# Kernel tuning notes

Hardware: AMD Instinct MI355X
Metric: run time of the kernel (lower is better)

## Reference

```python
import jax, jax.numpy as jnp
import numpy as np

N_OUT = 100000 - 1  # 99999, as hard-coded in the torch module
LEAK = 0.01         # torch LeakyReLU default slope


def setup_inputs() -> dict:
    key = jax.random.key(0)
    k1, k2, k3, k4, k5 = jax.random.split(key, 5)
    B, D = 512, 512
    H = D // 2
    x = jax.random.normal(k1, (B, D), dtype=jnp.float32)
    # torch.nn.Linear-style init scale ~ 1/sqrt(fan_in)
    w2 = jax.random.normal(k2, (H, D), dtype=jnp.float32) / np.sqrt(D)
    b2 = jax.random.normal(k3, (H,), dtype=jnp.float32) / np.sqrt(D)
    w3 = jax.random.normal(k4, (55, H), dtype=jnp.float32) / np.sqrt(H)
    b3 = jax.random.normal(k5, (55,), dtype=jnp.float32) / np.sqrt(H)
    return {"x": x, "w2": w2, "b2": b2, "w3": w3, "b3": b3}


def _digit_tables():
    # Static integer tables for i in [0, N_OUT).
    i = np.arange(N_OUT, dtype=np.int32)
    ndig = ((i >= 10).astype(np.int32) + (i >= 100) + (i >= 1000) + (i >= 10000)).astype(np.int32)
    ndig[0] = 1  # special case in the original code: i==0 -> n=1
    return jnp.asarray(i), jnp.asarray(ndig)


def reference(x, w2, b2, w3, b3):
    # tiny MLP (batched; equivalent to the per-sample torch loop)
    h = x @ w2.T + b2
    h = jnp.where(h >= 0, h, LEAK * h)          # LeakyReLU
    z = h @ w3.T + b3                            # [B, 55]
    p_len = jax.nn.softmax(z[:, :5], axis=-1)    # length distribution (5)
    p_dig = jax.nn.softmax(z[:, 5:].reshape(-1, 5, 10), axis=-1)  # 5 digit groups of 10
    x3 = jnp.concatenate([p_len, p_dig.reshape(-1, 50)], axis=-1)  # [B, 55]

    i, ndig = _digit_tables()                    # [N], [N]
    out = jnp.take(x3, ndig, axis=1)             # lead factor x3[k, n_i] -> [B, N]
    # Multiply the first n_i digit probabilities (original drops the last digit).
    for j in range(4):                           # max usable digits: n<=4
        expo = jnp.maximum(ndig - j, 0)
        d = (i // jnp.power(10, expo)) % 10      # j-th most significant digit
        idx = 5 + d + 10 * j                     # index into x3 digit groups
        factor = jnp.take(x3, idx, axis=1)       # [B, N]
        valid = (j < ndig)[None, :]
        out = out * jnp.where(valid, factor, 1.0)
    return out
```

## Files before the change

kernel.cpp:

```cpp
#include <hip/hip_runtime.h>
#include <hip/hip_bf16.h>


#define BATCH 512
#define DIM   512
#define HID   256
#define NCLS  55
#define NOUT  99999
#define RPB   4
#define LEAK  0.01f

__global__ __launch_bounds__(256) void mlp_x3_kernel(
    const float* __restrict__ x,  const float* __restrict__ w2,
    const float* __restrict__ b2, const float* __restrict__ w3,
    const float* __restrict__ b3, float* __restrict__ x3out) {
    __shared__ float xs[RPB][DIM];
    __shared__ float hs[RPB][HID];
    __shared__ float zs[RPB][NCLS];

    const int tid = threadIdx.x;
    const int k0  = blockIdx.x * RPB;

    for (int idx = tid; idx < RPB * DIM; idx += 256) {
        int r = idx >> 9;
        int d = idx & (DIM - 1);
        xs[r][d] = x[(k0 + r) * DIM + d];
    }
    __syncthreads();

    float acc[RPB];
#pragma unroll
    for (int r = 0; r < RPB; ++r) acc[r] = 0.f;
    const float* w2row = w2 + tid * DIM;
#pragma unroll 4
    for (int d = 0; d < DIM; ++d) {
        float w = w2row[d];
#pragma unroll
        for (int r = 0; r < RPB; ++r) acc[r] += w * xs[r][d];
    }
    float bb = b2[tid];
#pragma unroll
    for (int r = 0; r < RPB; ++r) {
        float hv = acc[r] + bb;
        hs[r][tid] = (hv >= 0.f) ? hv : LEAK * hv;
    }
    __syncthreads();

    if (tid < RPB * NCLS) {
        int r = tid / NCLS, o = tid % NCLS;
        const float* w3row = w3 + o * HID;
        float a = b3[o];
#pragma unroll 4
        for (int d = 0; d < HID; ++d) a += hs[r][d] * w3row[d];
        zs[r][o] = a;
    }
    __syncthreads();

    if (tid < RPB * 6) {
        int r = tid / 6, g = tid % 6;
        int off = (g == 0) ? 0 : 5 + 10 * (g - 1);
        int len = (g == 0) ? 5 : 10;
        float m = -1e30f;
        for (int u = 0; u < len; ++u) m = fmaxf(m, zs[r][off + u]);
        float s = 0.f;
        for (int u = 0; u < len; ++u) {
            float e = __expf(zs[r][off + u] - m);
            zs[r][off + u] = e;
            s += e;
        }
        float inv = 1.f / s;
        float* orow = x3out + (k0 + r) * NCLS + off;
        for (int u = 0; u < len; ++u) orow[u] = zs[r][off + u] * inv;
    }
}

__global__ __launch_bounds__(256) void expand_kernel(
    const float* __restrict__ x3, float* __restrict__ out, int ngroups) {
    int g = blockIdx.x * 256 + threadIdx.x;
    if (g >= ngroups) return;
    unsigned e0 = (unsigned)g * 4u;
    float vv[4];
#pragma unroll
    for (int u = 0; u < 4; ++u) {
        unsigned e = e0 + (unsigned)u;
        unsigned k = e / 99999u;
        unsigned i = e - k * 99999u;
        const float* row = x3 + k * (unsigned)NCLS;
        unsigned nd = (i >= 10u) + (i >= 100u) + (i >= 1000u) + (i >= 10000u);
        if (i == 0u) nd = 1u;
        float v;
        unsigned d1, d2, d3, d4, r;
        switch (nd) {
            case 0:
                v = row[0];
                break;
            case 1:
                d1 = i / 10u;
                v = row[1] * row[5 + d1];
                break;
            case 2:
                d2 = i / 100u; r = i - d2 * 100u; d1 = r / 10u;
                v = row[2] * row[5 + d2] * row[15 + d1];
                break;
            case 3:
                d3 = i / 1000u; r = i - d3 * 1000u;
                d2 = r / 100u; r -= d2 * 100u; d1 = r / 10u;
                v = row[3] * row[5 + d3] * row[15 + d2] * row[25 + d1];
                break;
            default:
                d4 = i / 10000u; r = i - d4 * 10000u;
                d3 = r / 1000u; r -= d3 * 1000u;
                d2 = r / 100u;  r -= d2 * 100u;  d1 = r / 10u;
                v = row[4] * row[5 + d4] * row[15 + d3] * row[25 + d2] * row[35 + d1];
                break;
        }
        vv[u] = v;
    }
    float4 res = make_float4(vv[0], vv[1], vv[2], vv[3]);
    ((float4*)out)[g] = res;
}

extern "C" void kernel_launch(void* const* d_in, const int* in_sizes, int n_in,
                              void* d_out, int out_size, void* d_ws, size_t ws_size,
                              hipStream_t stream) {
    const float* x  = (const float*)d_in[0];
    const float* w2 = (const float*)d_in[1];
    const float* b2 = (const float*)d_in[2];
    const float* w3 = (const float*)d_in[3];
    const float* b3 = (const float*)d_in[4];
    float* out = (float*)d_out;
    float* x3  = (float*)d_ws;

    mlp_x3_kernel<<<BATCH / RPB, 256, 0, stream>>>(x, w2, b2, w3, b3, x3);

    const int ngroups = (BATCH * NOUT) / 4;
    expand_kernel<<<(ngroups + 255) / 256, 256, 0, stream>>>(x3, out, ngroups);
}
```

Before: 268.1 us.

## Fuse MLP and expansion into one per-row kernel with precomputed product tables

Result: faster. 244.0 us (-9.0%).

```diff
diff --git a/kernel.cpp b/kernel.cpp
--- a/kernel.cpp
+++ b/kernel.cpp
@@ -7,117 +7,135 @@
 #define HID   256
 #define NCLS  55
 #define NOUT  99999
-#define RPB   4
 #define LEAK  0.01f
 
-__global__ __launch_bounds__(256) void mlp_x3_kernel(
+__device__ __forceinline__ float digit_factor(
+    unsigned i, const float* __restrict__ T4A, const float* __restrict__ T3A,
+    const float* __restrict__ T2A, const float* __restrict__ B4,
+    const float* __restrict__ B3, const float* __restrict__ A1x, float row0) {
+    if (i >= 10000u) {
+        unsigned t = i / 10u;
+        unsigned q = t / 100u;
+        unsigned r = t - q * 100u;
+        return T4A[q] * B4[r];
+    } else if (i >= 1000u) {
+        unsigned t = i / 10u;
+        unsigned q = t / 10u;
+        unsigned d = t - q * 10u;
+        return T3A[q] * B3[d];
+    } else if (i >= 100u) {
+        return T2A[i / 10u];
+    } else if (i >= 10u || i == 0u) {
+        return A1x[i / 10u];
+    }
+    return row0;
+}
+
+__global__ __launch_bounds__(256) void fused_mlp_expand(
     const float* __restrict__ x,  const float* __restrict__ w2,
     const float* __restrict__ b2, const float* __restrict__ w3,
-    const float* __restrict__ b3, float* __restrict__ x3out) {
-    __shared__ float xs[RPB][DIM];
-    __shared__ float hs[RPB][HID];
-    __shared__ float zs[RPB][NCLS];
+    const float* __restrict__ b3, float* __restrict__ out) {
+    __shared__ float xs[DIM];
+    __shared__ float hs[HID];
+    __shared__ float zp[4][NCLS];
+    __shared__ float x3s[NCLS];
+    __shared__ float T4A[100], T3A[100], T2A[100], B4[100];
+    __shared__ float B3[10], A1x[10];
 
     const int tid = threadIdx.x;
-    const int k0  = blockIdx.x * RPB;
+    const int k   = blockIdx.x;
 
-    for (int idx = tid; idx < RPB * DIM; idx += 256) {
-        int r = idx >> 9;
-        int d = idx & (DIM - 1);
-        xs[r][d] = x[(k0 + r) * DIM + d];
+    xs[tid]       = x[(size_t)k * DIM + tid];
+    xs[tid + 256] = x[(size_t)k * DIM + tid + 256];
+    __syncthreads();
+
+    {
+        const float4* w2r = (const float4*)(w2 + (size_t)tid * DIM);
+        const float4* xr  = (const float4*)xs;
+        float acc = 0.f;
+#pragma unroll 8
+        for (int d4 = 0; d4 < DIM / 4; ++d4) {
+            float4 w  = w2r[d4];
+            float4 xv = xr[d4];
+            acc += w.x * xv.x + w.y * xv.y + w.z * xv.z + w.w * xv.w;
+        }
+        acc += b2[tid];
+        hs[tid] = (acc >= 0.f) ? acc : LEAK * acc;
     }
     __syncthreads();
 
-    float acc[RPB];
+    if (tid < 4 * NCLS) {
+        int o = tid % NCLS, part = tid / NCLS;
+        const float4* w3r = (const float4*)(w3 + (size_t)o * HID + part * 64);
+        const float4* hr  = (const float4*)(hs + part * 64);
+        float a = 0.f;
 #pragma unroll
-    for (int r = 0; r < RPB; ++r) acc[r] = 0.f;
-    const float* w2row = w2 + tid * DIM;
-#pragma unroll 4
-    for (int d = 0; d < DIM; ++d) {
-        float w = w2row[d];
-#pragma unroll
-        for (int r = 0; r < RPB; ++r) acc[r] += w * xs[r][d];
+        for (int d4 = 0; d4 < 16; ++d4) {
+            float4 w = w3r[d4];
+            float4 h = hr[d4];
+            a += w.x * h.x + w.y * h.y + w.z * h.z + w.w * h.w;
+        }
+        zp[part][o] = a;
     }
-    float bb = b2[tid];
-#pragma unroll
-    for (int r = 0; r < RPB; ++r) {
-        float hv = acc[r] + bb;
-        hs[r][tid] = (hv >= 0.f) ? hv : LEAK * hv;
+    __syncthreads();
+    if (tid < NCLS)
+        x3s[tid] = zp[0][tid] + zp[1][tid] + zp[2][tid] + zp[3][tid] + b3[tid];
+    __syncthreads();
+
+    if (tid < 6) {
+        int off = (tid == 0) ? 0 : 5 + 10 * (tid - 1);
+        int len = (tid == 0) ? 5 : 10;
+        float m = -1e30f;
+        for (int u = 0; u < len; ++u) m = fmaxf(m, x3s[off + u]);
+        float s = 0.f;
+        for (int u = 0; u < len; ++u) {
+            float e = __expf(x3s[off + u] - m);
+            x3s[off + u] = e;
+            s += e;
+        }
+        float inv = 1.f / s;
+        for (int u = 0; u < len; ++u) x3s[off + u] *= inv;
     }
     __syncthreads();
 
-    if (tid < RPB * NCLS) {
-        int r = tid / NCLS, o = tid % NCLS;
-        const float* w3row = w3 + o * HID;
-        float a = b3[o];
-#pragma unroll 4
-        for (int d = 0; d < HID; ++d) a += hs[r][d] * w3row[d];
-        zs[r][o] = a;
+    for (int q = tid; q < 100; q += 256) {
+        int hi = q / 10, lo = q % 10;
+        float pp = x3s[5 + hi] * x3s[15 + lo];
+        T4A[q] = x3s[4] * pp;
+        T3A[q] = x3s[3] * pp;
+        T2A[q] = x3s[2] * pp;
+        B4[q]  = x3s[25 + hi] * x3s[35 + lo];
+    }
+    if (tid < 10) {
+        B3[tid]  = x3s[25 + tid];
+        A1x[tid] = x3s[1] * x3s[5 + tid];
     }
     __syncthreads();
 
-    if (tid < RPB * 6) {
-        int r = tid / 6, g = tid % 6;
-        int off = (g == 0) ? 0 : 5 + 10 * (g - 1);
-        int len = (g == 0) ? 5 : 10;
-        float m = -1e30f;
-        for (int u = 0; u < len; ++u) m = fmaxf(m, zs[r][off + u]);
-        float s = 0.f;
-        for (int u = 0; u < len; ++u) {
-            float e = __expf(zs[r][off + u] - m);
-            zs[r][off + u] = e;
-            s += e;
-        }
-        float inv = 1.f / s;
-        float* orow = x3out + (k0 + r) * NCLS + off;
-        for (int u = 0; u < len; ++u) orow[u] = zs[r][off + u] * inv;
+    const float row0 = x3s[0];
+
+    const size_t base = (size_t)k * NOUT;
+    const unsigned head = (unsigned)((4 - (base & 3)) & 3);
+    const unsigned ng = (NOUT - head) >> 2;
+    const unsigned tail_start = head + (ng << 2);
+
+    if (tid < (int)head)
+        out[base + tid] = digit_factor((unsigned)tid, T4A, T3A, T2A, B4, B3, A1x, row0);
+    if (tid < (int)(NOUT - tail_start)) {
+        unsigned i = tail_start + (unsigned)tid;
+        out[base + i] = digit_factor(i, T4A, T3A, T2A, B4, B3, A1x, row0);
     }
-}
 
-__global__ __launch_bounds__(256) void expand_kernel(
-    const float* __restrict__ x3, float* __restrict__ out, int ngroups) {
-    int g = blockIdx.x * 256 + threadIdx.x;
-    if (g >= ngroups) return;
-    unsigned e0 = (unsigned)g * 4u;
-    float vv[4];
-#pragma unroll
-    for (int u = 0; u < 4; ++u) {
-        unsigned e = e0 + (unsigned)u;
-        unsigned k = e / 99999u;
-        unsigned i = e - k * 99999u;
-        const float* row = x3 + k * (unsigned)NCLS;
-        unsigned nd = (i >= 10u) + (i >= 100u) + (i >= 1000u) + (i >= 10000u);
-        if (i == 0u) nd = 1u;
-        float v;
-        unsigned d1, d2, d3, d4, r;
-        switch (nd) {
-            case 0:
-                v = row[0];
-                break;
-            case 1:
-                d1 = i / 10u;
-                v = row[1] * row[5 + d1];
-                break;
-            case 2:
-                d2 = i / 100u; r = i - d2 * 100u; d1 = r / 10u;
-                v = row[2] * row[5 + d2] * row[15 + d1];
-                break;
-            case 3:
-                d3 = i / 1000u; r = i - d3 * 1000u;
-                d2 = r / 100u; r -= d2 * 100u; d1 = r / 10u;
-                v = row[3] * row[5 + d3] * row[15 + d2] * row[25 + d1];
-                break;
-            default:
-                d4 = i / 10000u; r = i - d4 * 10000u;
-                d3 = r / 1000u; r -= d3 * 1000u;
-                d2 = r / 100u;  r -= d2 * 100u;  d1 = r / 10u;
-                v = row[4] * row[5 + d4] * row[15 + d3] * row[25 + d2] * row[35 + d1];
-                break;
-        }
-        vv[u] = v;
+    float4* outv = (float4*)(out + base + head);
+    for (unsigned g = tid; g < ng; g += 256) {
+        unsigned i0 = head + (g << 2);
+        float4 v;
+        v.x = digit_factor(i0,      T4A, T3A, T2A, B4, B3, A1x, row0);
+        v.y = digit_factor(i0 + 1u, T4A, T3A, T2A, B4, B3, A1x, row0);
+        v.z = digit_factor(i0 + 2u, T4A, T3A, T2A, B4, B3, A1x, row0);
+        v.w = digit_factor(i0 + 3u, T4A, T3A, T2A, B4, B3, A1x, row0);
+        outv[g] = v;
     }
-    float4 res = make_float4(vv[0], vv[1], vv[2], vv[3]);
-    ((float4*)out)[g] = res;
 }
 
 extern "C" void kernel_launch(void* const* d_in, const int* in_sizes, int n_in,
@@ -129,10 +147,6 @@
     const float* w3 = (const float*)d_in[3];
     const float* b3 = (const float*)d_in[4];
     float* out = (float*)d_out;
-    float* x3  = (float*)d_ws;
 
-    mlp_x3_kernel<<<BATCH / RPB, 256, 0, stream>>>(x, w2, b2, w3, b3, x3);
-
-    const int ngroups = (BATCH * NOUT) / 4;
-    expand_kernel<<<(ngroups + 255) / 256, 256, 0, stream>>>(x3, out, ngroups);
+    fused_mlp_expand<<<BATCH, 256, 0, stream>>>(x, w2, b2, w3, b3, out);
 }
```
